# Kernel tuning notes

Measured on AMD Instinct MI355X. Metric: run time of the kernel, lower is better.

Reference implementation:

```python
import jax, jax.numpy as jnp
import numpy as np

N, E, G = 16384, 131072, 32
EPS = 1e-5


def seg_sum(x, ids, n):
    return jax.ops.segment_sum(x, ids, num_segments=n)


def seg_max(x, ids, n):
    return jax.ops.segment_max(x, ids, num_segments=n)


def gcn_conv(x, w, b, src, dst, n):
    # PyG GCNConv: add self loops, symmetric deg normalization
    loop = jnp.arange(n)
    s = jnp.concatenate([src, loop])
    d = jnp.concatenate([dst, loop])
    deg = seg_sum(jnp.ones_like(d, dtype=x.dtype), d, n)
    dis = jax.lax.rsqrt(deg)
    h = x @ w
    norm = (dis[s] * dis[d])[:, None]
    return seg_sum(h[s] * norm, d, n) + b


def sage_conv(x, wl, wr, b, src, dst, n):
    # mean aggregation of source features into target nodes
    cnt = seg_sum(jnp.ones_like(dst, dtype=x.dtype), dst, n)
    agg = seg_sum(x[src], dst, n) / jnp.maximum(cnt, 1.0)[:, None]
    return agg @ wl + x @ wr + b


def gat_conv(x, w, a_src, a_dst, b, src, dst, n, heads=4, ch=256):
    loop = jnp.arange(n)
    s = jnp.concatenate([src, loop])
    d = jnp.concatenate([dst, loop])
    h = (x @ w).reshape(n, heads, ch)            # [N,H,C]
    es = jnp.sum(h * a_src, axis=-1)             # [N,H]
    ed = jnp.sum(h * a_dst, axis=-1)             # [N,H]
    e = jax.nn.leaky_relu(es[s] + ed[d], 0.2)    # [E2,H]
    m = seg_max(e, d, n)
    ex = jnp.exp(e - m[d])
    z = seg_sum(ex, d, n)
    alpha = ex / z[d]                            # softmax over incoming edges
    out = seg_sum(h[s] * alpha[:, :, None], d, n)  # [N,H,C]
    return out.mean(axis=1) + b                  # concat=False -> head mean


def batchnorm(x, g, b):
    mu = x.mean(axis=0)
    var = x.var(axis=0)
    return (x - mu) * jax.lax.rsqrt(var + EPS) * g + b


def setup_inputs() -> dict:
    key = jax.random.key(0)
    ks = jax.random.split(key, 16)
    def w(k, shape, fan_in):
        return jax.random.normal(k, shape, jnp.float32) * (1.0 / np.sqrt(fan_in))
    return {
        "x": jax.random.uniform(ks[0], (N, 5), jnp.float32),
        "edge_index": jax.random.randint(ks[1], (2, E), 0, N),
        "batch": jnp.sort(jax.random.randint(ks[2], (N,), 0, G)),
        "gcn1_w": w(ks[3], (5, 64), 5), "gcn1_b": jnp.zeros((64,), jnp.float32),
        "sage_wl": w(ks[4], (64, 128), 64), "sage_wr": w(ks[5], (64, 128), 64),
        "sage_b": jnp.zeros((128,), jnp.float32),
        "gat_w": w(ks[6], (128, 1024), 128),
        "gat_asrc": w(ks[7], (4, 256), 256), "gat_adst": w(ks[8], (4, 256), 256),
        "gat_b": jnp.zeros((256,), jnp.float32),
        "gcn4_w": w(ks[9], (256, 512), 256), "gcn4_b": jnp.zeros((512,), jnp.float32),
        "bn1_g": jnp.ones((64,), jnp.float32), "bn1_b": jnp.zeros((64,), jnp.float32),
        "bn2_g": jnp.ones((128,), jnp.float32), "bn2_b": jnp.zeros((128,), jnp.float32),
        "bn3_g": jnp.ones((256,), jnp.float32), "bn3_b": jnp.zeros((256,), jnp.float32),
        "bn4_g": jnp.ones((512,), jnp.float32), "bn4_b": jnp.zeros((512,), jnp.float32),
        "fc_w": w(ks[10], (1024, 1024), 1024), "fc_b": jnp.zeros((1024,), jnp.float32),
    }


def reference(x, edge_index, batch, gcn1_w, gcn1_b, sage_wl, sage_wr, sage_b,
              gat_w, gat_asrc, gat_adst, gat_b, gcn4_w, gcn4_b,
              bn1_g, bn1_b, bn2_g, bn2_b, bn3_g, bn3_b, bn4_g, bn4_b,
              fc_w, fc_b):
    src, dst = edge_index[0], edge_index[1]
    n = x.shape[0]
    h = jax.nn.relu(batchnorm(gcn_conv(x, gcn1_w, gcn1_b, src, dst, n), bn1_g, bn1_b))
    h = jax.nn.relu(batchnorm(sage_conv(h, sage_wl, sage_wr, sage_b, src, dst, n), bn2_g, bn2_b))
    h = jax.nn.relu(batchnorm(gat_conv(h, gat_w, gat_asrc, gat_adst, gat_b, src, dst, n), bn3_g, bn3_b))
    h = jax.nn.relu(batchnorm(gcn_conv(h, gcn4_w, gcn4_b, src, dst, n), bn4_g, bn4_b))
    # global mean / max pooling over graphs in the batch
    cnt = seg_sum(jnp.ones((n,), h.dtype), batch, G)
    mean_p = seg_sum(h, batch, G) / jnp.maximum(cnt, 1.0)[:, None]
    max_p = seg_max(h, batch, G)
    max_p = jnp.where(cnt[:, None] > 0, max_p, 0.0)
    pooled = jnp.concatenate([mean_p, max_p], axis=1)  # [G,1024]
    return pooled @ fc_w + fc_b
```

## Files before the change

### kernel.cpp

```cpp
#include <hip/hip_runtime.h>

#define N_ 16384
#define E_ 131072
#define G_ 32
#define EPSF 1e-5f

typedef unsigned short bf16u;
typedef __attribute__((ext_vector_type(8))) short s8v;
typedef __attribute__((ext_vector_type(4))) float f4v;

__device__ __forceinline__ bf16u f2bf(float v) {
    union { float f; unsigned u; } x; x.f = v;
    unsigned r = x.u + 0x7FFF + ((x.u >> 16) & 1);
    return (bf16u)(r >> 16);
}
__device__ __forceinline__ float bf2f(bf16u u) {
    union { unsigned u; float f; } x; x.u = (unsigned)u << 16;
    return x.f;
}

static const size_t OFF_INDEG = 0;
static const size_t OFF_BNS   = 65536;
static const size_t OFF_BNQ   = 131072;
static const size_t OFF_POOL  = 196608;
static const size_t OFF_GB    = 327680;
static const size_t OFF_CNT   = 327816;
static const size_t OFF_MSET  = 327936;
static const size_t OFF_ROWS  = 327936;
static const size_t OFF_CURSOR= 393728;
static const size_t OFF_CSR   = 459264;
static const size_t OFF_DIS   = 983552;
static const size_t OFF_ES    = 1049088;
static const size_t OFF_ED    = 1311232;
static const size_t OFF_PART  = 1573376;
static const size_t OFF_BN1C  = 1578496;
static const size_t OFF_XA    = 1786624;
static const size_t OFF_AB    = 5980928;
static const size_t OFF_H2P   = 10175232;
static const size_t OFF_H2B   = 14369536;
static const size_t OFF_H3B   = 18563840;
static const size_t OFF_AGG   = 35328768;
static const size_t OFF_XA4B  = 52105984;
static const size_t OFF_WT1   = 68883200;
static const size_t OFF_WT2   = 69145344;
static const size_t OFF_WT3   = 69407488;
static const size_t OFF_H4B   = 69440256;
static const size_t OFF_VES   = 86479616;
static const size_t OFF_VED   = 86481664;

__global__ __launch_bounds__(1024) void k_scan(const int* __restrict__ indeg,
                                               int* __restrict__ rows,
                                               int* __restrict__ cursor,
                                               float* __restrict__ dis) {
    __shared__ int wtot[16];
    int t = threadIdx.x;
    int lane = t & 63, wave = t >> 6;
    int base = t * 16;
    int local[16];
    int s = 0;
#pragma unroll
    for (int i = 0; i < 16; ++i) {
        local[i] = indeg[base + i]; s += local[i];
        dis[base + i] = rsqrtf((float)local[i] + 1.0f);
    }
    int own = s;
#pragma unroll
    for (int off = 1; off < 64; off <<= 1) {
        int v = __shfl_up(s, off, 64);
        if (lane >= off) s += v;
    }
    if (lane == 63) wtot[wave] = s;
    __syncthreads();
    if (wave == 0) {
        int v = (lane < 16) ? wtot[lane] : 0;
#pragma unroll
        for (int off = 1; off < 16; off <<= 1) {
            int u = __shfl_up(v, off, 64);
            if (lane >= off) v += u;
        }
        if (lane < 16) wtot[lane] = v;
    }
    __syncthreads();
    int run = s - own + (wave > 0 ? wtot[wave - 1] : 0);
#pragma unroll
    for (int i = 0; i < 16; ++i) {
        rows[base + i] = run; cursor[base + i] = run; run += local[i];
    }
    if (t == 1023) rows[N_] = run;
}

__global__ void k_fill(const int* __restrict__ src, const int* __restrict__ dst,
                       int* __restrict__ cursor, int* __restrict__ csr) {
    int e = blockIdx.x * 256 + threadIdx.x;
    if (e < E_) {
        int p = atomicAdd(&cursor[dst[e]], 1);
        csr[p] = src[e];
    }
}

__global__ void k_wconv_all(const float* __restrict__ gat_w,
                            const float* __restrict__ gcn4_w,
                            const float* __restrict__ wl, const float* __restrict__ wr,
                            const int* __restrict__ batch,
                            const float* __restrict__ gat_as,
                            const float* __restrict__ gat_ad,
                            const int* __restrict__ dstE,
                            bf16u* __restrict__ wT1, bf16u* __restrict__ wT2,
                            bf16u* __restrict__ wT3, int* __restrict__ gb,
                            float* __restrict__ ves, float* __restrict__ ved,
                            int* __restrict__ indeg) {
    int idx = blockIdx.x * 256 + threadIdx.x;
    if (idx < 131072) {
        int k = idx >> 10, col = idx & 1023;
        int h = col >> 8, c = col & 255;
        wT1[(size_t)c * 512 + h * 128 + k] = f2bf(0.25f * gat_w[idx]);
    } else if (idx < 262144) {
        int j = idx - 131072;
        int k = j >> 9, m = j & 511;
        wT2[m * 256 + k] = f2bf(gcn4_w[j]);
    } else if (idx < 270336) {
        int j = idx - 262144;
        int k = j >> 7, m = j & 127;
        wT3[m * 128 + k] = f2bf(wl[j]);
    } else if (idx < 278528) {
        int j = idx - 270336;
        int k = j >> 7, m = j & 127;
        wT3[m * 128 + 64 + k] = f2bf(wr[j]);
    } else if (idx < 278592) {
        int g = idx - 278528;
        if (g > G_) return;
        if (g == G_) { gb[G_] = N_; return; }
        int lo = 0, hi = N_;
        while (lo < hi) { int mid = (lo + hi) >> 1; if (batch[mid] < g) lo = mid + 1; else hi = mid; }
        gb[g] = lo;
    } else if (idx < 279104) {
        int j = idx - 278592;
        int h = j >> 7, k = j & 127;
        float s = 0.f;
        for (int c = 0; c < 256; ++c)
            s += gat_w[(size_t)k * 1024 + h*256 + c] * gat_as[h*256 + c];
        ves[j] = s;
    } else if (idx < 279616) {
        int j = idx - 279104;
        int h = j >> 7, k = j & 127;
        float s = 0.f;
        for (int c = 0; c < 256; ++c)
            s += gat_w[(size_t)k * 1024 + h*256 + c] * gat_ad[h*256 + c];
        ved[j] = s;
    } else if (idx < 410688) {
        int e = idx - 279616;
        atomicAdd(&indeg[dstE[e]], 1);
    }
}

__global__ __launch_bounds__(256) void k_gcn1x(const float* __restrict__ x,
                                               const float* __restrict__ dis,
                                               const int* __restrict__ rows,
                                               const int* __restrict__ csr,
                                               float* __restrict__ xa) {
    int wave = threadIdx.x >> 6, lane = threadIdx.x & 63;
    int i = blockIdx.x * 4 + wave;
    float a0=0,a1=0,a2=0,a3=0,a4=0;
    int e0 = rows[i], e1 = rows[i+1];
    for (int e = e0 + lane; e < e1; e += 64) {
        int s = csr[e];
        float wt = dis[s];
        a0 += x[s*5+0]*wt; a1 += x[s*5+1]*wt; a2 += x[s*5+2]*wt;
        a3 += x[s*5+3]*wt; a4 += x[s*5+4]*wt;
    }
#pragma unroll
    for (int off = 32; off > 0; off >>= 1) {
        a0 += __shfl_xor(a0, off, 64); a1 += __shfl_xor(a1, off, 64);
        a2 += __shfl_xor(a2, off, 64); a3 += __shfl_xor(a3, off, 64);
        a4 += __shfl_xor(a4, off, 64);
    }
    float di = dis[i];
    float v0 = di*(a0 + di*x[i*5+0]);
    float v1 = di*(a1 + di*x[i*5+1]);
    float v2 = di*(a2 + di*x[i*5+2]);
    float v3 = di*(a3 + di*x[i*5+3]);
    float v4 = di*(a4 + di*x[i*5+4]);
    if (lane < 5) {
        float v = lane == 0 ? v0 : lane == 1 ? v1 : lane == 2 ? v2 : lane == 3 ? v3 : v4;
        xa[(size_t)i*8 + lane] = v;
    }
}

__global__ __launch_bounds__(256) void k_xstats(const float* __restrict__ xa,
                                                float* __restrict__ partial,
                                                int* __restrict__ cnt,
                                                const float* __restrict__ w,
                                                const float* __restrict__ b,
                                                const float* __restrict__ bng,
                                                const float* __restrict__ bnb,
                                                float* __restrict__ sc,
                                                float* __restrict__ sh) {
    __shared__ float wsum[80];
    __shared__ int lastFlag;
    int t = threadIdx.x;
    int tid = blockIdx.x * 256 + t;
    float v0 = xa[(size_t)tid*8+0], v1 = xa[(size_t)tid*8+1], v2 = xa[(size_t)tid*8+2];
    float v3 = xa[(size_t)tid*8+3], v4 = xa[(size_t)tid*8+4];
    float m[20];
    m[0]=v0; m[1]=v1; m[2]=v2; m[3]=v3; m[4]=v4;
    m[5]=v0*v0;  m[6]=v0*v1;  m[7]=v0*v2;  m[8]=v0*v3;  m[9]=v0*v4;
    m[10]=v1*v1; m[11]=v1*v2; m[12]=v1*v3; m[13]=v1*v4;
    m[14]=v2*v2; m[15]=v2*v3; m[16]=v2*v4;
    m[17]=v3*v3; m[18]=v3*v4;
    m[19]=v4*v4;
#pragma unroll
    for (int off = 32; off > 0; off >>= 1)
#pragma unroll
        for (int j = 0; j < 20; ++j) m[j] += __shfl_xor(m[j], off, 64);
    int wave = t >> 6, lane = t & 63;
    if (lane == 0)
#pragma unroll
        for (int j = 0; j < 20; ++j) wsum[wave*20 + j] = m[j];
    __syncthreads();
    if (t < 20) {
        partial[blockIdx.x * 20 + t] = wsum[t] + wsum[20+t] + wsum[40+t] + wsum[60+t];
        __threadfence();
    }
    __syncthreads();
    if (t == 0) lastFlag = (atomicAdd(cnt, 1) == 63);
    __syncthreads();
    if (!lastFlag || t >= 64) return;
    int l = t;
    const float invN = 1.0f / (float)N_;
    float mm[20];
#pragma unroll
    for (int j = 0; j < 20; ++j) {
        float v = partial[l*20 + j];
#pragma unroll
        for (int off = 32; off > 0; off >>= 1) v += __shfl_xor(v, off, 64);
        mm[j] = v * invN;
    }
    int c = l;
    float wc0 = w[c], wc1 = w[64+c], wc2 = w[128+c], wc3 = w[192+c], wc4 = w[256+c];
    float mu = b[c] + mm[0]*wc0 + mm[1]*wc1 + mm[2]*wc2 + mm[3]*wc3 + mm[4]*wc4;
    float var = 0.f;
    var += (mm[5]  - mm[0]*mm[0]) * wc0*wc0;
    var += (mm[6]  - mm[0]*mm[1]) * wc0*wc1 * 2.f;
    var += (mm[7]  - mm[0]*mm[2]) * wc0*wc2 * 2.f;
    var += (mm[8]  - mm[0]*mm[3]) * wc0*wc3 * 2.f;
    var += (mm[9]  - mm[0]*mm[4]) * wc0*wc4 * 2.f;
    var += (mm[10] - mm[1]*mm[1]) * wc1*wc1;
    var += (mm[11] - mm[1]*mm[2]) * wc1*wc2 * 2.f;
    var += (mm[12] - mm[1]*mm[3]) * wc1*wc3 * 2.f;
    var += (mm[13] - mm[1]*mm[4]) * wc1*wc4 * 2.f;
    var += (mm[14] - mm[2]*mm[2]) * wc2*wc2;
    var += (mm[15] - mm[2]*mm[3]) * wc2*wc3 * 2.f;
    var += (mm[16] - mm[2]*mm[4]) * wc2*wc4 * 2.f;
    var += (mm[17] - mm[3]*mm[3]) * wc3*wc3;
    var += (mm[18] - mm[3]*mm[4]) * wc3*wc4 * 2.f;
    var += (mm[19] - mm[4]*mm[4]) * wc4*wc4;
    float scale = rsqrtf(var + EPSF) * bng[c];
    sc[c] = scale;
    sh[c] = fmaf(b[c], scale, bnb[c] - mu * scale);
}

__global__ __launch_bounds__(256) void k_sage_l1(const float* __restrict__ xa,
                                                 const float* __restrict__ sc,
                                                 const float* __restrict__ sh,
                                                 const float* __restrict__ w,
                                                 const int* __restrict__ rows,
                                                 const int* __restrict__ csr,
                                                 bf16u* __restrict__ ab) {
    int wave = threadIdx.x >> 6, lane = threadIdx.x & 63;
    int i = blockIdx.x * 4 + wave;
    int c = lane;
    float wc0 = w[c], wc1 = w[64+c], wc2 = w[128+c], wc3 = w[192+c], wc4 = w[256+c];
    float scale = sc[c], base = sh[c];
    {
        float4 p = *(const float4*)&xa[(size_t)i*8];
        float p4 = xa[(size_t)i*8 + 4];
        float t = p.x*wc0 + p.y*wc1 + p.z*wc2 + p.w*wc3 + p4*wc4;
        float v = fmaf(t, scale, base); v = v > 0.f ? v : 0.f;
        ab[(size_t)i*128 + 64 + c] = f2bf(v);
    }
    int e0 = rows[i], e1 = rows[i+1];
    float s = 0.f;
    int e = e0;
    for (; e + 3 < e1; e += 4) {
        int s0 = csr[e], s1 = csr[e+1], s2 = csr[e+2], s3 = csr[e+3];
        float4 q0 = *(const float4*)&xa[(size_t)s0*8]; float r0 = xa[(size_t)s0*8+4];
        float4 q1 = *(const float4*)&xa[(size_t)s1*8]; float r1 = xa[(size_t)s1*8+4];
        float4 q2 = *(const float4*)&xa[(size_t)s2*8]; float r2 = xa[(size_t)s2*8+4];
        float4 q3 = *(const float4*)&xa[(size_t)s3*8]; float r3 = xa[(size_t)s3*8+4];
        float t0 = q0.x*wc0 + q0.y*wc1 + q0.z*wc2 + q0.w*wc3 + r0*wc4;
        float t1 = q1.x*wc0 + q1.y*wc1 + q1.z*wc2 + q1.w*wc3 + r1*wc4;
        float t2 = q2.x*wc0 + q2.y*wc1 + q2.z*wc2 + q2.w*wc3 + r2*wc4;
        float t3 = q3.x*wc0 + q3.y*wc1 + q3.z*wc2 + q3.w*wc3 + r3*wc4;
        float v;
        v = fmaf(t0, scale, base); s += v > 0.f ? v : 0.f;
        v = fmaf(t1, scale, base); s += v > 0.f ? v : 0.f;
        v = fmaf(t2, scale, base); s += v > 0.f ? v : 0.f;
        v = fmaf(t3, scale, base); s += v > 0.f ? v : 0.f;
    }
    for (; e < e1; ++e) {
        int sI = csr[e];
        float4 q = *(const float4*)&xa[(size_t)sI*8]; float r = xa[(size_t)sI*8+4];
        float t = q.x*wc0 + q.y*wc1 + q.z*wc2 + q.w*wc3 + r*wc4;
        float v = fmaf(t, scale, base); s += v > 0.f ? v : 0.f;
    }
    ab[(size_t)i*128 + c] = f2bf(s / fmaxf((float)(e1 - e0), 1.0f));
}

__global__ __launch_bounds__(256) void k_gemm_mfma(const bf16u* __restrict__ A,
                                                   const bf16u* __restrict__ BT,
                                                   const float* __restrict__ bias,
                                                   bf16u* __restrict__ C,
                                                   float* __restrict__ sum,
                                                   float* __restrict__ sumsq,
                                                   int K, int M) {
    __shared__ bf16u As[128][40];
    __shared__ bf16u Bs[128][40];
    int tid = threadIdx.x;
    int wave = tid >> 6, lane = tid & 63;
    int wr = (wave >> 1) * 64, wc = (wave & 1) * 64;
    int row0 = blockIdx.y * 128, col0 = blockIdx.x * 128;
    f4v acc[4][4];
#pragma unroll
    for (int i = 0; i < 4; ++i)
#pragma unroll
        for (int j = 0; j < 4; ++j) acc[i][j] = (f4v)0.0f;

    int sr = tid >> 1;
    int sh = (tid & 1) * 16;
    int lr = lane & 15, lq = lane >> 4;

    for (int k0 = 0; k0 < K; k0 += 32) {
        const bf16u* ap = A + (size_t)(row0 + sr) * K + k0 + sh;
        *(uint4*)&As[sr][sh]     = *(const uint4*)ap;
        *(uint4*)&As[sr][sh + 8] = *(const uint4*)(ap + 8);
        const bf16u* bp = BT + (size_t)(col0 + sr) * K + k0 + sh;
        *(uint4*)&Bs[sr][sh]     = *(const uint4*)bp;
        *(uint4*)&Bs[sr][sh + 8] = *(const uint4*)(bp + 8);
        __syncthreads();
        s8v af[4], bfr[4];
#pragma unroll
        for (int i = 0; i < 4; ++i)
            af[i] = *(const s8v*)&As[wr + i*16 + lr][lq*8];
#pragma unroll
        for (int j = 0; j < 4; ++j)
            bfr[j] = *(const s8v*)&Bs[wc + j*16 + lr][lq*8];
#pragma unroll
        for (int i = 0; i < 4; ++i)
#pragma unroll
            for (int j = 0; j < 4; ++j)
                acc[i][j] = __builtin_amdgcn_mfma_f32_16x16x32_bf16(af[i], bfr[j], acc[i][j], 0, 0, 0);
        __syncthreads();
    }

    int slot = (blockIdx.y & 7) << 9;
#pragma unroll
    for (int j = 0; j < 4; ++j) {
        int col = col0 + wc + j*16 + lr;
        float bv = bias ? bias[col] : 0.f;
        float s = 0.f, q = 0.f;
#pragma unroll
        for (int i = 0; i < 4; ++i) {
#pragma unroll
            for (int r = 0; r < 4; ++r) {
                float v = acc[i][j][r] + bv;
                int row = row0 + wr + i*16 + lq*4 + r;
                C[(size_t)row * M + col] = f2bf(v);
                s += v; q += v*v;
            }
        }
        if (sum) {
            s += __shfl_xor(s, 16, 64); q += __shfl_xor(q, 16, 64);
            s += __shfl_xor(s, 32, 64); q += __shfl_xor(q, 32, 64);
            if (lq == 0) { atomicAdd(&sum[slot + col], s); atomicAdd(&sumsq[slot + col], q); }
        }
    }
}

__global__ __launch_bounds__(256) void k_bn_apply2b_attn(
        const bf16u* __restrict__ hp, const float* __restrict__ sum,
        const float* __restrict__ sumsq, const float* __restrict__ g,
        const float* __restrict__ b, const float* __restrict__ ves,
        const float* __restrict__ ved, bf16u* __restrict__ hb,
        float* __restrict__ es, float* __restrict__ ed) {
    int wave = threadIdx.x >> 6, lane = threadIdx.x & 63;
    int i = blockIdx.x * 4 + wave;
    int c = lane * 2;
    const float invN = 1.0f / (float)N_;
    float sx=0.f, sy=0.f, qx=0.f, qy=0.f;
#pragma unroll
    for (int s8 = 0; s8 < 8; ++s8) {
        float2 a = *(const float2*)&sum[s8*512 + c];
        float2 d = *(const float2*)&sumsq[s8*512 + c];
        sx += a.x; sy += a.y; qx += d.x; qy += d.y;
    }
    float2 gg = *(const float2*)&g[c];
    float2 bb = *(const float2*)&b[c];
    float mu0 = sx*invN, mu1 = sy*invN;
    float sc0 = rsqrtf(qx*invN - mu0*mu0 + EPSF)*gg.x, sh0 = bb.x - mu0*sc0;
    float sc1 = rsqrtf(qy*invN - mu1*mu1 + EPSF)*gg.y, sh1 = bb.y - mu1*sc1;
    unsigned pv = *(const unsigned*)&hp[(size_t)i*128 + c];
    float v0 = bf2f((bf16u)(pv & 0xFFFF));
    float v1 = bf2f((bf16u)(pv >> 16));
    v0 = fmaf(v0, sc0, sh0); v0 = v0 > 0.f ? v0 : 0.f;
    v1 = fmaf(v1, sc1, sh1); v1 = v1 > 0.f ? v1 : 0.f;
    unsigned ow = (unsigned)f2bf(v0) | ((unsigned)f2bf(v1) << 16);
    *(unsigned*)&hb[(size_t)i*128 + c] = ow;
    float vs[4], vd[4];
#pragma unroll
    for (int h = 0; h < 4; ++h) {
        float2 a = *(const float2*)&ves[h*128 + c];
        float2 d = *(const float2*)&ved[h*128 + c];
        vs[h] = v0*a.x + v1*a.y;
        vd[h] = v0*d.x + v1*d.y;
    }
#pragma unroll
    for (int off = 32; off > 0; off >>= 1) {
#pragma unroll
        for (int h = 0; h < 4; ++h) {
            vs[h] += __shfl_xor(vs[h], off, 64);
            vd[h] += __shfl_xor(vd[h], off, 64);
        }
    }
    if (lane == 0) {
        *(float4*)&es[i*4] = make_float4(vs[0], vs[1], vs[2], vs[3]);
        *(float4*)&ed[i*4] = make_float4(vd[0], vd[1], vd[2], vd[3]);
    }
}

__global__ __launch_bounds__(256) void k_gat_agg2(const bf16u* __restrict__ h2b,
                                                  const float* __restrict__ es,
                                                  const float* __restrict__ ed,
                                                  const int* __restrict__ rows,
                                                  const int* __restrict__ csr,
                                                  bf16u* __restrict__ agg) {
    int wave = threadIdx.x >> 6, lane = threadIdx.x & 63;
    int i = blockIdx.x * 4 + wave;
    int c = lane * 2;
    float4 edv = *(const float4*)&ed[i*4];
    float4 sv  = *(const float4*)&es[i*4];
    int e0 = rows[i], e1 = rows[i+1];
    float e, m0, m1, m2, m3;
    e = sv.x + edv.x; m0 = e >= 0.f ? e : 0.2f*e;
    e = sv.y + edv.y; m1 = e >= 0.f ? e : 0.2f*e;
    e = sv.z + edv.z; m2 = e >= 0.f ? e : 0.2f*e;
    e = sv.w + edv.w; m3 = e >= 0.f ? e : 0.2f*e;
    float z0, z1, z2, z3;
    float a00, a01, a10, a11, a20, a21, a30, a31;
    {
        z0 = 1.f; z1 = 1.f; z2 = 1.f; z3 = 1.f;
        unsigned pv = *(const unsigned*)&h2b[(size_t)i*128 + c];
        float v0 = bf2f((bf16u)(pv & 0xFFFF)), v1 = bf2f((bf16u)(pv >> 16));
        a00 = v0; a01 = v1; a10 = v0; a11 = v1;
        a20 = v0; a21 = v1; a30 = v0; a31 = v1;
    }
#define GEXP(Q, EDC, M) __expf(fminf(((Q) + (EDC) >= 0.f ? (Q) + (EDC) : 0.2f*((Q) + (EDC))) - (M), 80.f))
    int ee = e0;
    for (; ee + 3 < e1; ee += 4) {
        int s0 = csr[ee], s1 = csr[ee+1], s2i = csr[ee+2], s3i = csr[ee+3];
        float4 q0 = *(const float4*)&es[s0*4];
        float4 q1 = *(const float4*)&es[s1*4];
        float4 q2 = *(const float4*)&es[s2i*4];
        float4 q3 = *(const float4*)&es[s3i*4];
        unsigned p0 = *(const unsigned*)&h2b[(size_t)s0*128 + c];
        unsigned p1 = *(const unsigned*)&h2b[(size_t)s1*128 + c];
        unsigned p2 = *(const unsigned*)&h2b[(size_t)s2i*128 + c];
        unsigned p3 = *(const unsigned*)&h2b[(size_t)s3i*128 + c];
        float v0, v1, ex;
        v0 = bf2f((bf16u)(p0 & 0xFFFF)); v1 = bf2f((bf16u)(p0 >> 16));
        ex = GEXP(q0.x, edv.x, m0); z0 += ex; a00 = fmaf(ex, v0, a00); a01 = fmaf(ex, v1, a01);
        ex = GEXP(q0.y, edv.y, m1); z1 += ex; a10 = fmaf(ex, v0, a10); a11 = fmaf(ex, v1, a11);
        ex = GEXP(q0.z, edv.z, m2); z2 += ex; a20 = fmaf(ex, v0, a20); a21 = fmaf(ex, v1, a21);
        ex = GEXP(q0.w, edv.w, m3); z3 += ex; a30 = fmaf(ex, v0, a30); a31 = fmaf(ex, v1, a31);
        v0 = bf2f((bf16u)(p1 & 0xFFFF)); v1 = bf2f((bf16u)(p1 >> 16));
        ex = GEXP(q1.x, edv.x, m0); z0 += ex; a00 = fmaf(ex, v0, a00); a01 = fmaf(ex, v1, a01);
        ex = GEXP(q1.y, edv.y, m1); z1 += ex; a10 = fmaf(ex, v0, a10); a11 = fmaf(ex, v1, a11);
        ex = GEXP(q1.z, edv.z, m2); z2 += ex; a20 = fmaf(ex, v0, a20); a21 = fmaf(ex, v1, a21);
        ex = GEXP(q1.w, edv.w, m3); z3 += ex; a30 = fmaf(ex, v0, a30); a31 = fmaf(ex, v1, a31);
        v0 = bf2f((bf16u)(p2 & 0xFFFF)); v1 = bf2f((bf16u)(p2 >> 16));
        ex = GEXP(q2.x, edv.x, m0); z0 += ex; a00 = fmaf(ex, v0, a00); a01 = fmaf(ex, v1, a01);
        ex = GEXP(q2.y, edv.y, m1); z1 += ex; a10 = fmaf(ex, v0, a10); a11 = fmaf(ex, v1, a11);
        ex = GEXP(q2.z, edv.z, m2); z2 += ex; a20 = fmaf(ex, v0, a20); a21 = fmaf(ex, v1, a21);
        ex = GEXP(q2.w, edv.w, m3); z3 += ex; a30 = fmaf(ex, v0, a30); a31 = fmaf(ex, v1, a31);
        v0 = bf2f((bf16u)(p3 & 0xFFFF)); v1 = bf2f((bf16u)(p3 >> 16));
        ex = GEXP(q3.x, edv.x, m0); z0 += ex; a00 = fmaf(ex, v0, a00); a01 = fmaf(ex, v1, a01);
        ex = GEXP(q3.y, edv.y, m1); z1 += ex; a10 = fmaf(ex, v0, a10); a11 = fmaf(ex, v1, a11);
        ex = GEXP(q3.z, edv.z, m2); z2 += ex; a20 = fmaf(ex, v0, a20); a21 = fmaf(ex, v1, a21);
        ex = GEXP(q3.w, edv.w, m3); z3 += ex; a30 = fmaf(ex, v0, a30); a31 = fmaf(ex, v1, a31);
    }
    for (; ee < e1; ++ee) {
        int s = csr[ee];
        float4 s2 = *(const float4*)&es[s*4];
        unsigned pv = *(const unsigned*)&h2b[(size_t)s*128 + c];
        float v0 = bf2f((bf16u)(pv & 0xFFFF)), v1 = bf2f((bf16u)(pv >> 16));
        float ex;
        ex = GEXP(s2.x, edv.x, m0); z0 += ex; a00 = fmaf(ex, v0, a00); a01 = fmaf(ex, v1, a01);
        ex = GEXP(s2.y, edv.y, m1); z1 += ex; a10 = fmaf(ex, v0, a10); a11 = fmaf(ex, v1, a11);
        ex = GEXP(s2.z, edv.z, m2); z2 += ex; a20 = fmaf(ex, v0, a20); a21 = fmaf(ex, v1, a21);
        ex = GEXP(s2.w, edv.w, m3); z3 += ex; a30 = fmaf(ex, v0, a30); a31 = fmaf(ex, v1, a31);
    }
#undef GEXP
    size_t base = (size_t)i * 512 + c;
    float r; unsigned ow;
    r = 1.f/z0; ow = (unsigned)f2bf(a00*r) | ((unsigned)f2bf(a01*r) << 16);
    *(unsigned*)&agg[base]       = ow;
    r = 1.f/z1; ow = (unsigned)f2bf(a10*r) | ((unsigned)f2bf(a11*r) << 16);
    *(unsigned*)&agg[base + 128] = ow;
    r = 1.f/z2; ow = (unsigned)f2bf(a20*r) | ((unsigned)f2bf(a21*r) << 16);
    *(unsigned*)&agg[base + 256] = ow;
    r = 1.f/z3; ow = (unsigned)f2bf(a30*r) | ((unsigned)f2bf(a31*r) << 16);
    *(unsigned*)&agg[base + 384] = ow;
}

__global__ __launch_bounds__(256) void k_gcn4_agg(const bf16u* __restrict__ h3b,
                                                  const float* __restrict__ dis,
                                                  const int* __restrict__ rows,
                                                  const int* __restrict__ csr,
                                                  const float* __restrict__ sum,
                                                  const float* __restrict__ sumsq,
                                                  const float* __restrict__ g,
                                                  const float* __restrict__ b,
                                                  bf16u* __restrict__ xab) {
    int wave = threadIdx.x >> 6, q = threadIdx.x & 63;
    int i = blockIdx.x * 4 + wave;
    int c = q * 4;
    const float invN = 1.0f / (float)N_;
    float4 sm = make_float4(0.f,0.f,0.f,0.f), sq = make_float4(0.f,0.f,0.f,0.f);
#pragma unroll
    for (int s8 = 0; s8 < 8; ++s8) {
        float4 a = *(const float4*)&sum[s8*512 + c];
        float4 d = *(const float4*)&sumsq[s8*512 + c];
        sm.x += a.x; sm.y += a.y; sm.z += a.z; sm.w += a.w;
        sq.x += d.x; sq.y += d.y; sq.z += d.z; sq.w += d.w;
    }
    float4 gg = *(const float4*)&g[c];
    float4 bb = *(const float4*)&b[c];
    float mu, sc0, sc1, sc2, sc3, sh0, sh1, sh2, sh3;
    mu = sm.x*invN; sc0 = rsqrtf(sq.x*invN - mu*mu + EPSF)*gg.x; sh0 = bb.x - mu*sc0;
    mu = sm.y*invN; sc1 = rsqrtf(sq.y*invN - mu*mu + EPSF)*gg.y; sh1 = bb.y - mu*sc1;
    mu = sm.z*invN; sc2 = rsqrtf(sq.z*invN - mu*mu + EPSF)*gg.z; sh2 = bb.z - mu*sc2;
    mu = sm.w*invN; sc3 = rsqrtf(sq.w*invN - mu*mu + EPSF)*gg.w; sh3 = bb.w - mu*sc3;
    float di = dis[i];
    float a0, a1, a2, a3;
    {
        ushort4 u = *(const ushort4*)(h3b + (size_t)i*256 + c);
        float v, dd = di * di;
        v = fmaf(bf2f(u.x), sc0, sh0); v = v > 0.f ? v : 0.f; a0 = v * dd;
        v = fmaf(bf2f(u.y), sc1, sh1); v = v > 0.f ? v : 0.f; a1 = v * dd;
        v = fmaf(bf2f(u.z), sc2, sh2); v = v > 0.f ? v : 0.f; a2 = v * dd;
        v = fmaf(bf2f(u.w), sc3, sh3); v = v > 0.f ? v : 0.f; a3 = v * dd;
    }
    int e0 = rows[i], e1 = rows[i+1];
    int e = e0;
    for (; e + 3 < e1; e += 4) {
        int s0 = csr[e], s1 = csr[e+1], s2i = csr[e+2], s3i = csr[e+3];
        float w0 = dis[s0] * di, w1 = dis[s1] * di, w2 = dis[s2i] * di, w3 = dis[s3i] * di;
        ushort4 u0 = *(const ushort4*)(h3b + (size_t)s0*256 + c);
        ushort4 u1 = *(const ushort4*)(h3b + (size_t)s1*256 + c);
        ushort4 u2 = *(const ushort4*)(h3b + (size_t)s2i*256 + c);
        ushort4 u3 = *(const ushort4*)(h3b + (size_t)s3i*256 + c);
        float v;
        v = fmaf(bf2f(u0.x), sc0, sh0); v = v > 0.f ? v : 0.f; a0 += v * w0;
        v = fmaf(bf2f(u0.y), sc1, sh1); v = v > 0.f ? v : 0.f; a1 += v * w0;
        v = fmaf(bf2f(u0.z), sc2, sh2); v = v > 0.f ? v : 0.f; a2 += v * w0;
        v = fmaf(bf2f(u0.w), sc3, sh3); v = v > 0.f ? v : 0.f; a3 += v * w0;
        v = fmaf(bf2f(u1.x), sc0, sh0); v = v > 0.f ? v : 0.f; a0 += v * w1;
        v = fmaf(bf2f(u1.y), sc1, sh1); v = v > 0.f ? v : 0.f; a1 += v * w1;
        v = fmaf(bf2f(u1.z), sc2, sh2); v = v > 0.f ? v : 0.f; a2 += v * w1;
        v = fmaf(bf2f(u1.w), sc3, sh3); v = v > 0.f ? v : 0.f; a3 += v * w1;
        v = fmaf(bf2f(u2.x), sc0, sh0); v = v > 0.f ? v : 0.f; a0 += v * w2;
        v = fmaf(bf2f(u2.y), sc1, sh1); v = v > 0.f ? v : 0.f; a1 += v * w2;
        v = fmaf(bf2f(u2.z), sc2, sh2); v = v > 0.f ? v : 0.f; a2 += v * w2;
        v = fmaf(bf2f(u2.w), sc3, sh3); v = v > 0.f ? v : 0.f; a3 += v * w2;
        v = fmaf(bf2f(u3.x), sc0, sh0); v = v > 0.f ? v : 0.f; a0 += v * w3;
        v = fmaf(bf2f(u3.y), sc1, sh1); v = v > 0.f ? v : 0.f; a1 += v * w3;
        v = fmaf(bf2f(u3.z), sc2, sh2); v = v > 0.f ? v : 0.f; a2 += v * w3;
        v = fmaf(bf2f(u3.w), sc3, sh3); v = v > 0.f ? v : 0.f; a3 += v * w3;
    }
    for (; e < e1; ++e) {
        int s = csr[e];
        float w = dis[s] * di;
        ushort4 u = *(const ushort4*)(h3b + (size_t)s*256 + c);
        float v;
        v = fmaf(bf2f(u.x), sc0, sh0); v = v > 0.f ? v : 0.f; a0 += v * w;
        v = fmaf(bf2f(u.y), sc1, sh1); v = v > 0.f ? v : 0.f; a1 += v * w;
        v = fmaf(bf2f(u.z), sc2, sh2); v = v > 0.f ? v : 0.f; a2 += v * w;
        v = fmaf(bf2f(u.w), sc3, sh3); v = v > 0.f ? v : 0.f; a3 += v * w;
    }
    ushort4 o;
    o.x = f2bf(a0); o.y = f2bf(a1); o.z = f2bf(a2); o.w = f2bf(a3);
    *(ushort4*)(xab + (size_t)i*256 + c) = o;
}

__global__ void k_pool(const bf16u* __restrict__ h4b, const int* __restrict__ gb,
                       const float* __restrict__ sum, const float* __restrict__ sumsq,
                       const float* __restrict__ g, const float* __restrict__ b,
                       const float* __restrict__ fcb,
                       float* __restrict__ pooled, float* __restrict__ out) {
    int bidx = blockIdx.x;
    int t = threadIdx.x;
    if (bidx >= 512) {
        int i = (bidx - 512) * 256 + t;
        out[i] = fcb[i & 1023];
        return;
    }
    int gi = bidx >> 4;
    int chunk = bidx & 15;
    const float invN = 1.0f / (float)N_;
    float su0=0.f, qq0=0.f, su1=0.f, qq1=0.f;
#pragma unroll
    for (int s8 = 0; s8 < 8; ++s8) {
        su0 += sum[s8*512 + t];       qq0 += sumsq[s8*512 + t];
        su1 += sum[s8*512 + 256 + t]; qq1 += sumsq[s8*512 + 256 + t];
    }
    float mu0 = su0 * invN;
    float sc0 = rsqrtf(qq0 * invN - mu0*mu0 + EPSF) * g[t];
    float sh0 = b[t] - mu0 * sc0;
    float mu1 = su1 * invN;
    float sc1 = rsqrtf(qq1 * invN - mu1*mu1 + EPSF) * g[t+256];
    float sh1 = b[t+256] - mu1 * sc1;
    int r0g = gb[gi], r1g = gb[gi+1];
    int n = r1g - r0g;
    if (n <= 0) return;
    int per = (n + 15) >> 4;
    int r0 = r0g + chunk * per;
    int r1 = min(r0 + per, r1g);
    if (r0 >= r1) return;
    float s0=0.f, s1=0.f, m0=0.f, m1=0.f;
    for (int r = r0; r < r1; ++r) {
        float v = fmaf(bf2f(h4b[(size_t)r*512 + t]), sc0, sh0);
        v = v > 0.f ? v : 0.f;
        s0 += v; m0 = fmaxf(m0, v);
        float w = fmaf(bf2f(h4b[(size_t)r*512 + 256 + t]), sc1, sh1);
        w = w > 0.f ? w : 0.f;
        s1 += w; m1 = fmaxf(m1, w);
    }
    atomicAdd(&pooled[gi*1024 + t], s0);
    atomicAdd(&pooled[gi*1024 + 256 + t], s1);
    atomicMax((int*)&pooled[gi*1024 + 512 + t],  __float_as_int(m0));
    atomicMax((int*)&pooled[gi*1024 + 768 + t],  __float_as_int(m1));
}

#define FCKZ 16
#define FCKC (1024 / FCKZ)

__global__ __launch_bounds__(256) void k_fc2(const float* __restrict__ pooled,
                                             const float* __restrict__ w,
                                             const int* __restrict__ gb,
                                             float* __restrict__ out) {
    __shared__ float pr[FCKC];
    int g = blockIdx.x;
    int z = blockIdx.y;
    int t = threadIdx.x;
    int k0 = z * FCKC;
    if (t < FCKC) {
        float scale = (z < 8) ? 1.0f / fmaxf((float)(gb[g+1] - gb[g]), 1.0f) : 1.0f;
        pr[t] = pooled[g * 1024 + k0 + t] * scale;
    }
    __syncthreads();
    int m0 = t * 4;
    float ax = 0.f, ay = 0.f, az = 0.f, aw = 0.f;
#pragma unroll 8
    for (int k = 0; k < FCKC; ++k) {
        const float4 wv = *(const float4*)&w[(size_t)(k0 + k) * 1024 + m0];
        float p = pr[k];
        ax += p * wv.x; ay += p * wv.y; az += p * wv.z; aw += p * wv.w;
    }
    atomicAdd(&out[g * 1024 + m0 + 0], ax);
    atomicAdd(&out[g * 1024 + m0 + 1], ay);
    atomicAdd(&out[g * 1024 + m0 + 2], az);
    atomicAdd(&out[g * 1024 + m0 + 3], aw);
}

extern "C" void kernel_launch(void* const* d_in, const int* in_sizes, int n_in,
                              void* d_out, int out_size, void* d_ws, size_t ws_size,
                              hipStream_t stream) {
    (void)in_sizes; (void)n_in; (void)out_size; (void)ws_size;
    const float* x       = (const float*)d_in[0];
    const int*   ei      = (const int*)d_in[1];
    const int*   batch   = (const int*)d_in[2];
    const float* gcn1_w  = (const float*)d_in[3];
    const float* gcn1_b  = (const float*)d_in[4];
    const float* sage_wl = (const float*)d_in[5];
    const float* sage_wr = (const float*)d_in[6];
    const float* sage_b  = (const float*)d_in[7];
    const float* gat_w   = (const float*)d_in[8];
    const float* gat_as  = (const float*)d_in[9];
    const float* gat_ad  = (const float*)d_in[10];
    const float* gat_b   = (const float*)d_in[11];
    const float* gcn4_w  = (const float*)d_in[12];
    const float* gcn4_b  = (const float*)d_in[13];
    const float* bn1_g   = (const float*)d_in[14];
    const float* bn1_b   = (const float*)d_in[15];
    const float* bn2_g   = (const float*)d_in[16];
    const float* bn2_b   = (const float*)d_in[17];
    const float* bn3_g   = (const float*)d_in[18];
    const float* bn3_b   = (const float*)d_in[19];
    const float* bn4_g   = (const float*)d_in[20];
    const float* bn4_b   = (const float*)d_in[21];
    const float* fc_w    = (const float*)d_in[22];
    const float* fc_b    = (const float*)d_in[23];
    float* out = (float*)d_out;

    char* w8 = (char*)d_ws;
    int*   indeg  = (int*)(w8 + OFF_INDEG);
    float* bns    = (float*)(w8 + OFF_BNS);
    float* bnq    = (float*)(w8 + OFF_BNQ);
    float* pooled = (float*)(w8 + OFF_POOL);
    int*   gb     = (int*)(w8 + OFF_GB);
    int*   cnt    = (int*)(w8 + OFF_CNT);
    int*   rows   = (int*)(w8 + OFF_ROWS);
    int*   cursor = (int*)(w8 + OFF_CURSOR);
    int*   csr    = (int*)(w8 + OFF_CSR);
    float* dis    = (float*)(w8 + OFF_DIS);
    float* es     = (float*)(w8 + OFF_ES);
    float* ed     = (float*)(w8 + OFF_ED);
    float* part   = (float*)(w8 + OFF_PART);
    float* bn1sc  = (float*)(w8 + OFF_BN1C);
    float* bn1sh  = (float*)(w8 + OFF_BN1C + 256);
    float* xa     = (float*)(w8 + OFF_XA);
    bf16u* ab     = (bf16u*)(w8 + OFF_AB);
    bf16u* h2p    = (bf16u*)(w8 + OFF_H2P);
    bf16u* h2b    = (bf16u*)(w8 + OFF_H2B);
    bf16u* h3b    = (bf16u*)(w8 + OFF_H3B);
    bf16u* agg    = (bf16u*)(w8 + OFF_AGG);
    bf16u* xa4b   = (bf16u*)(w8 + OFF_XA4B);
    bf16u* wT1    = (bf16u*)(w8 + OFF_WT1);
    bf16u* wT2    = (bf16u*)(w8 + OFF_WT2);
    bf16u* wT3    = (bf16u*)(w8 + OFF_WT3);
    bf16u* h4b    = (bf16u*)(w8 + OFF_H4B);
    float* ves    = (float*)(w8 + OFF_VES);
    float* ved    = (float*)(w8 + OFF_VED);

    const int* srcE = ei;
    const int* dstE = ei + E_;

    hipMemsetAsync(w8, 0, OFF_MSET, stream);
    k_wconv_all<<<1605, 256, 0, stream>>>(gat_w, gcn4_w, sage_wl, sage_wr, batch,
                                          gat_as, gat_ad, dstE,
                                          wT1, wT2, wT3, gb, ves, ved, indeg);
    k_scan<<<1, 1024, 0, stream>>>(indeg, rows, cursor, dis);
    k_fill<<<E_/256, 256, 0, stream>>>(srcE, dstE, cursor, csr);

    k_gcn1x<<<N_/4, 256, 0, stream>>>(x, dis, rows, csr, xa);
    k_xstats<<<64, 256, 0, stream>>>(xa, part, cnt, gcn1_w, gcn1_b, bn1_g, bn1_b,
                                     bn1sc, bn1sh);
    k_sage_l1<<<N_/4, 256, 0, stream>>>(xa, bn1sc, bn1sh, gcn1_w, rows, csr, ab);

    {
        dim3 grid(1, N_/128);
        k_gemm_mfma<<<grid, 256, 0, stream>>>(ab, wT3, sage_b, h2p,
                                              bns + 4096, bnq + 4096, 128, 128);
    }
    k_bn_apply2b_attn<<<N_/4, 256, 0, stream>>>(h2p, bns + 4096, bnq + 4096, bn2_g, bn2_b,
                                                ves, ved, h2b, es, ed);

    k_gat_agg2<<<N_/4, 256, 0, stream>>>(h2b, es, ed, rows, csr, agg);
    {
        dim3 grid(256/128, N_/128);
        k_gemm_mfma<<<grid, 256, 0, stream>>>(agg, wT1, gat_b, h3b,
                                              bns + 8192, bnq + 8192, 512, 256);
    }

    k_gcn4_agg<<<N_/4, 256, 0, stream>>>(h3b, dis, rows, csr, bns + 8192, bnq + 8192,
                                         bn3_g, bn3_b, xa4b);
    {
        dim3 grid(512/128, N_/128);
        k_gemm_mfma<<<grid, 256, 0, stream>>>(xa4b, wT2, gcn4_b, h4b,
                                              bns + 12288, bnq + 12288, 256, 512);
    }

    k_pool<<<640, 256, 0, stream>>>(h4b, gb, bns + 12288, bnq + 12288, bn4_g, bn4_b,
                                    fc_b, pooled, out);

    {
        dim3 grid(G_, FCKZ);
        k_fc2<<<grid, 256, 0, stream>>>(pooled, fc_w, gb, out);
    }
}
```

Baseline: 285.5 us.

## Fuse indegree count with scan, CSR fill with weight prep, stats into gcn1

Merges five front-end kernels into three. The indegree atomic count now carries the prefix scan in its last block, selected by an atomic counter. The CSR fill shares a launch with the weight conversion. The BN1 statistics reduction moves into the gcn1 aggregation kernel using a last-block pattern. The intent is to remove launch and inter-kernel gaps. In exchange the scan runs in a single 256-thread block doing serial 64-element loops, and the stats finalisation reads 4096 partials in one block.

New measurement: 394.0 us. 1.38x slower.

```diff
diff --git a/kernel.cpp b/kernel.cpp
--- a/kernel.cpp
+++ b/kernel.cpp
@@ -25,6 +25,7 @@
 static const size_t OFF_POOL  = 196608;
 static const size_t OFF_GB    = 327680;
 static const size_t OFF_CNT   = 327816;
+static const size_t OFF_CNT2  = 327820;
 static const size_t OFF_MSET  = 327936;
 static const size_t OFF_ROWS  = 327936;
 static const size_t OFF_CURSOR= 393728;
@@ -33,83 +34,84 @@
 static const size_t OFF_ES    = 1049088;
 static const size_t OFF_ED    = 1311232;
 static const size_t OFF_PART  = 1573376;
-static const size_t OFF_BN1C  = 1578496;
-static const size_t OFF_XA    = 1786624;
-static const size_t OFF_AB    = 5980928;
-static const size_t OFF_H2P   = 10175232;
-static const size_t OFF_H2B   = 14369536;
-static const size_t OFF_H3B   = 18563840;
-static const size_t OFF_AGG   = 35328768;
-static const size_t OFF_XA4B  = 52105984;
-static const size_t OFF_WT1   = 68883200;
-static const size_t OFF_WT2   = 69145344;
-static const size_t OFF_WT3   = 69407488;
-static const size_t OFF_H4B   = 69440256;
-static const size_t OFF_VES   = 86479616;
-static const size_t OFF_VED   = 86481664;
-
-__global__ __launch_bounds__(1024) void k_scan(const int* __restrict__ indeg,
+static const size_t OFF_BN1C  = 1901056;
+static const size_t OFF_XA    = 1901568;
+static const size_t OFF_AB    = 2425856;
+static const size_t OFF_H2P   = 6620160;
+static const size_t OFF_H2B   = 10814464;
+static const size_t OFF_H3B   = 15008768;
+static const size_t OFF_AGG   = 23397376;
+static const size_t OFF_XA4B  = 40174592;
+static const size_t OFF_WT1   = 48563200;
+static const size_t OFF_WT2   = 48825344;
+static const size_t OFF_WT3   = 49087488;
+static const size_t OFF_H4B   = 49120256;
+static const size_t OFF_VES   = 65897472;
+static const size_t OFF_VED   = 65899520;
+
+__global__ __launch_bounds__(256) void k_indeg(const int* __restrict__ dstE,
+                                               int* __restrict__ indeg,
+                                               int* __restrict__ cnt,
                                                int* __restrict__ rows,
                                                int* __restrict__ cursor,
                                                float* __restrict__ dis) {
-    __shared__ int wtot[16];
+    __shared__ int lpart[256];
+    __shared__ int lastFlag;
     int t = threadIdx.x;
-    int lane = t & 63, wave = t >> 6;
-    int base = t * 16;
-    int local[16];
+    int e = blockIdx.x * 256 + t;
+    atomicAdd(&indeg[dstE[e]], 1);
+    __threadfence();
+    __syncthreads();
+    if (t == 0) lastFlag = (atomicAdd(cnt, 1) == 511);
+    __syncthreads();
+    if (!lastFlag) return;
+    __threadfence();
+    int base = t * 64;
     int s = 0;
-#pragma unroll
-    for (int i = 0; i < 16; ++i) {
-        local[i] = indeg[base + i]; s += local[i];
-        dis[base + i] = rsqrtf((float)local[i] + 1.0f);
-    }
-    int own = s;
-#pragma unroll
-    for (int off = 1; off < 64; off <<= 1) {
-        int v = __shfl_up(s, off, 64);
-        if (lane >= off) s += v;
-    }
-    if (lane == 63) wtot[wave] = s;
-    __syncthreads();
-    if (wave == 0) {
-        int v = (lane < 16) ? wtot[lane] : 0;
-#pragma unroll
-        for (int off = 1; off < 16; off <<= 1) {
-            int u = __shfl_up(v, off, 64);
-            if (lane >= off) v += u;
-        }
-        if (lane < 16) wtot[lane] = v;
-    }
-    __syncthreads();
-    int run = s - own + (wave > 0 ? wtot[wave - 1] : 0);
-#pragma unroll
-    for (int i = 0; i < 16; ++i) {
-        rows[base + i] = run; cursor[base + i] = run; run += local[i];
-    }
-    if (t == 1023) rows[N_] = run;
-}
-
-__global__ void k_fill(const int* __restrict__ src, const int* __restrict__ dst,
-                       int* __restrict__ cursor, int* __restrict__ csr) {
-    int e = blockIdx.x * 256 + threadIdx.x;
-    if (e < E_) {
-        int p = atomicAdd(&cursor[dst[e]], 1);
-        csr[p] = src[e];
-    }
-}
-
-__global__ void k_wconv_all(const float* __restrict__ gat_w,
-                            const float* __restrict__ gcn4_w,
-                            const float* __restrict__ wl, const float* __restrict__ wr,
-                            const int* __restrict__ batch,
-                            const float* __restrict__ gat_as,
-                            const float* __restrict__ gat_ad,
-                            const int* __restrict__ dstE,
-                            bf16u* __restrict__ wT1, bf16u* __restrict__ wT2,
-                            bf16u* __restrict__ wT3, int* __restrict__ gb,
-                            float* __restrict__ ves, float* __restrict__ ved,
-                            int* __restrict__ indeg) {
-    int idx = blockIdx.x * 256 + threadIdx.x;
+    for (int i = 0; i < 64; ++i) s += indeg[base + i];
+    lpart[t] = s;
+    __syncthreads();
+    for (int off = 1; off < 256; off <<= 1) {
+        int v = (t >= off) ? lpart[t - off] : 0;
+        __syncthreads();
+        lpart[t] += v;
+        __syncthreads();
+    }
+    int run = (t == 0) ? 0 : lpart[t - 1];
+    for (int i = 0; i < 64; ++i) {
+        int d = indeg[base + i];
+        rows[base + i] = run; cursor[base + i] = run;
+        dis[base + i] = rsqrtf((float)d + 1.0f);
+        run += d;
+    }
+    if (t == 255) rows[N_] = run;
+}
+
+__global__ __launch_bounds__(256) void k_fillw(const int* __restrict__ srcE,
+                                               const int* __restrict__ dstE,
+                                               int* __restrict__ cursor,
+                                               int* __restrict__ csr,
+                                               const float* __restrict__ gat_w,
+                                               const float* __restrict__ gcn4_w,
+                                               const float* __restrict__ wl,
+                                               const float* __restrict__ wr,
+                                               const int* __restrict__ batch,
+                                               const float* __restrict__ gat_as,
+                                               const float* __restrict__ gat_ad,
+                                               bf16u* __restrict__ wT1,
+                                               bf16u* __restrict__ wT2,
+                                               bf16u* __restrict__ wT3,
+                                               int* __restrict__ gb,
+                                               float* __restrict__ ves,
+                                               float* __restrict__ ved) {
+    int bid = blockIdx.x, t = threadIdx.x;
+    if (bid < 512) {
+        int e = bid * 256 + t;
+        int p = atomicAdd(&cursor[dstE[e]], 1);
+        csr[p] = srcE[e];
+        return;
+    }
+    int idx = (bid - 512) * 256 + t;
     if (idx < 131072) {
         int k = idx >> 10, col = idx & 1023;
         int h = col >> 8, c = col & 255;
@@ -147,9 +149,6 @@
         for (int c = 0; c < 256; ++c)
             s += gat_w[(size_t)k * 1024 + h*256 + c] * gat_ad[h*256 + c];
         ved[j] = s;
-    } else if (idx < 410688) {
-        int e = idx - 279616;
-        atomicAdd(&indeg[dstE[e]], 1);
     }
 }
 
@@ -157,8 +156,19 @@
                                                const float* __restrict__ dis,
                                                const int* __restrict__ rows,
                                                const int* __restrict__ csr,
-                                               float* __restrict__ xa) {
-    int wave = threadIdx.x >> 6, lane = threadIdx.x & 63;
+                                               float* __restrict__ xa,
+                                               float* __restrict__ partial,
+                                               int* __restrict__ cnt2,
+                                               const float* __restrict__ w,
+                                               const float* __restrict__ b,
+                                               const float* __restrict__ bng,
+                                               const float* __restrict__ bnb,
+                                               float* __restrict__ sc,
+                                               float* __restrict__ sh) {
+    __shared__ float wm[80];
+    __shared__ int lastFlag;
+    int t = threadIdx.x;
+    int wave = t >> 6, lane = t & 63;
     int i = blockIdx.x * 4 + wave;
     float a0=0,a1=0,a2=0,a3=0,a4=0;
     int e0 = rows[i], e1 = rows[i+1];
@@ -184,79 +194,70 @@
         float v = lane == 0 ? v0 : lane == 1 ? v1 : lane == 2 ? v2 : lane == 3 ? v3 : v4;
         xa[(size_t)i*8 + lane] = v;
     }
-}
-
-__global__ __launch_bounds__(256) void k_xstats(const float* __restrict__ xa,
-                                                float* __restrict__ partial,
-                                                int* __restrict__ cnt,
-                                                const float* __restrict__ w,
-                                                const float* __restrict__ b,
-                                                const float* __restrict__ bng,
-                                                const float* __restrict__ bnb,
-                                                float* __restrict__ sc,
-                                                float* __restrict__ sh) {
-    __shared__ float wsum[80];
-    __shared__ int lastFlag;
-    int t = threadIdx.x;
-    int tid = blockIdx.x * 256 + t;
-    float v0 = xa[(size_t)tid*8+0], v1 = xa[(size_t)tid*8+1], v2 = xa[(size_t)tid*8+2];
-    float v3 = xa[(size_t)tid*8+3], v4 = xa[(size_t)tid*8+4];
-    float m[20];
-    m[0]=v0; m[1]=v1; m[2]=v2; m[3]=v3; m[4]=v4;
-    m[5]=v0*v0;  m[6]=v0*v1;  m[7]=v0*v2;  m[8]=v0*v3;  m[9]=v0*v4;
-    m[10]=v1*v1; m[11]=v1*v2; m[12]=v1*v3; m[13]=v1*v4;
-    m[14]=v2*v2; m[15]=v2*v3; m[16]=v2*v4;
-    m[17]=v3*v3; m[18]=v3*v4;
-    m[19]=v4*v4;
+    if (lane == 0) {
+        wm[wave*20 + 0] = v0;  wm[wave*20 + 1] = v1;  wm[wave*20 + 2] = v2;
+        wm[wave*20 + 3] = v3;  wm[wave*20 + 4] = v4;
+        wm[wave*20 + 5] = v0*v0;  wm[wave*20 + 6] = v0*v1;  wm[wave*20 + 7] = v0*v2;
+        wm[wave*20 + 8] = v0*v3;  wm[wave*20 + 9] = v0*v4;
+        wm[wave*20 +10] = v1*v1;  wm[wave*20 +11] = v1*v2;  wm[wave*20 +12] = v1*v3;
+        wm[wave*20 +13] = v1*v4;
+        wm[wave*20 +14] = v2*v2;  wm[wave*20 +15] = v2*v3;  wm[wave*20 +16] = v2*v4;
+        wm[wave*20 +17] = v3*v3;  wm[wave*20 +18] = v3*v4;
+        wm[wave*20 +19] = v4*v4;
+    }
+    __syncthreads();
+    if (t < 20) {
+        partial[blockIdx.x * 20 + t] = wm[t] + wm[20+t] + wm[40+t] + wm[60+t];
+        __threadfence();
+    }
+    __syncthreads();
+    if (t == 0) lastFlag = (atomicAdd(cnt2, 1) == 4095);
+    __syncthreads();
+    if (!lastFlag) return;
+    __threadfence();
+    float mm[20];
+#pragma unroll
+    for (int j = 0; j < 20; ++j) mm[j] = 0.f;
+    for (int r = t; r < 4096; r += 256) {
+#pragma unroll
+        for (int j = 0; j < 20; ++j) mm[j] += partial[r*20 + j];
+    }
 #pragma unroll
     for (int off = 32; off > 0; off >>= 1)
 #pragma unroll
-        for (int j = 0; j < 20; ++j) m[j] += __shfl_xor(m[j], off, 64);
-    int wave = t >> 6, lane = t & 63;
+        for (int j = 0; j < 20; ++j) mm[j] += __shfl_xor(mm[j], off, 64);
+    __syncthreads();
     if (lane == 0)
 #pragma unroll
-        for (int j = 0; j < 20; ++j) wsum[wave*20 + j] = m[j];
-    __syncthreads();
-    if (t < 20) {
-        partial[blockIdx.x * 20 + t] = wsum[t] + wsum[20+t] + wsum[40+t] + wsum[60+t];
-        __threadfence();
-    }
-    __syncthreads();
-    if (t == 0) lastFlag = (atomicAdd(cnt, 1) == 63);
-    __syncthreads();
-    if (!lastFlag || t >= 64) return;
-    int l = t;
-    const float invN = 1.0f / (float)N_;
-    float mm[20];
-#pragma unroll
-    for (int j = 0; j < 20; ++j) {
-        float v = partial[l*20 + j];
-#pragma unroll
-        for (int off = 32; off > 0; off >>= 1) v += __shfl_xor(v, off, 64);
-        mm[j] = v * invN;
-    }
-    int c = l;
-    float wc0 = w[c], wc1 = w[64+c], wc2 = w[128+c], wc3 = w[192+c], wc4 = w[256+c];
-    float mu = b[c] + mm[0]*wc0 + mm[1]*wc1 + mm[2]*wc2 + mm[3]*wc3 + mm[4]*wc4;
-    float var = 0.f;
-    var += (mm[5]  - mm[0]*mm[0]) * wc0*wc0;
-    var += (mm[6]  - mm[0]*mm[1]) * wc0*wc1 * 2.f;
-    var += (mm[7]  - mm[0]*mm[2]) * wc0*wc2 * 2.f;
-    var += (mm[8]  - mm[0]*mm[3]) * wc0*wc3 * 2.f;
-    var += (mm[9]  - mm[0]*mm[4]) * wc0*wc4 * 2.f;
-    var += (mm[10] - mm[1]*mm[1]) * wc1*wc1;
-    var += (mm[11] - mm[1]*mm[2]) * wc1*wc2 * 2.f;
-    var += (mm[12] - mm[1]*mm[3]) * wc1*wc3 * 2.f;
-    var += (mm[13] - mm[1]*mm[4]) * wc1*wc4 * 2.f;
-    var += (mm[14] - mm[2]*mm[2]) * wc2*wc2;
-    var += (mm[15] - mm[2]*mm[3]) * wc2*wc3 * 2.f;
-    var += (mm[16] - mm[2]*mm[4]) * wc2*wc4 * 2.f;
-    var += (mm[17] - mm[3]*mm[3]) * wc3*wc3;
-    var += (mm[18] - mm[3]*mm[4]) * wc3*wc4 * 2.f;
-    var += (mm[19] - mm[4]*mm[4]) * wc4*wc4;
-    float scale = rsqrtf(var + EPSF) * bng[c];
-    sc[c] = scale;
-    sh[c] = fmaf(b[c], scale, bnb[c] - mu * scale);
+        for (int j = 0; j < 20; ++j) wm[wave*20 + j] = mm[j];
+    __syncthreads();
+    if (t < 20) wm[t] = (wm[t] + wm[20+t] + wm[40+t] + wm[60+t]) * (1.0f/(float)N_);
+    __syncthreads();
+    if (t < 64) {
+        int c = t;
+        float M0=wm[0], M1=wm[1], M2=wm[2], M3=wm[3], M4=wm[4];
+        float wc0 = w[c], wc1 = w[64+c], wc2 = w[128+c], wc3 = w[192+c], wc4 = w[256+c];
+        float mu = b[c] + M0*wc0 + M1*wc1 + M2*wc2 + M3*wc3 + M4*wc4;
+        float var = 0.f;
+        var += (wm[5]  - M0*M0) * wc0*wc0;
+        var += (wm[6]  - M0*M1) * wc0*wc1 * 2.f;
+        var += (wm[7]  - M0*M2) * wc0*wc2 * 2.f;
+        var += (wm[8]  - M0*M3) * wc0*wc3 * 2.f;
+        var += (wm[9]  - M0*M4) * wc0*wc4 * 2.f;
+        var += (wm[10] - M1*M1) * wc1*wc1;
+        var += (wm[11] - M1*M2) * wc1*wc2 * 2.f;
+        var += (wm[12] - M1*M3) * wc1*wc3 * 2.f;
+        var += (wm[13] - M1*M4) * wc1*wc4 * 2.f;
+        var += (wm[14] - M2*M2) * wc2*wc2;
+        var += (wm[15] - M2*M3) * wc2*wc3 * 2.f;
+        var += (wm[16] - M2*M4) * wc2*wc4 * 2.f;
+        var += (wm[17] - M3*M3) * wc3*wc3;
+        var += (wm[18] - M3*M4) * wc3*wc4 * 2.f;
+        var += (wm[19] - M4*M4) * wc4*wc4;
+        float scale = rsqrtf(var + EPSF) * bng[c];
+        sc[c] = scale;
+        sh[c] = fmaf(b[c], scale, bnb[c] - mu * scale);
+    }
 }
 
 __global__ __launch_bounds__(256) void k_sage_l1(const float* __restrict__ xa,
@@ -708,6 +709,7 @@
     float* pooled = (float*)(w8 + OFF_POOL);
     int*   gb     = (int*)(w8 + OFF_GB);
     int*   cnt    = (int*)(w8 + OFF_CNT);
+    int*   cnt2   = (int*)(w8 + OFF_CNT2);
     int*   rows   = (int*)(w8 + OFF_ROWS);
     int*   cursor = (int*)(w8 + OFF_CURSOR);
     int*   csr    = (int*)(w8 + OFF_CSR);
@@ -735,15 +737,13 @@
     const int* dstE = ei + E_;
 
     hipMemsetAsync(w8, 0, OFF_MSET, stream);
-    k_wconv_all<<<1605, 256, 0, stream>>>(gat_w, gcn4_w, sage_wl, sage_wr, batch,
-                                          gat_as, gat_ad, dstE,
-                                          wT1, wT2, wT3, gb, ves, ved, indeg);
-    k_scan<<<1, 1024, 0, stream>>>(indeg, rows, cursor, dis);
-    k_fill<<<E_/256, 256, 0, stream>>>(srcE, dstE, cursor, csr);
-
-    k_gcn1x<<<N_/4, 256, 0, stream>>>(x, dis, rows, csr, xa);
-    k_xstats<<<64, 256, 0, stream>>>(xa, part, cnt, gcn1_w, gcn1_b, bn1_g, bn1_b,
-                                     bn1sc, bn1sh);
+    k_indeg<<<512, 256, 0, stream>>>(dstE, indeg, cnt, rows, cursor, dis);
+    k_fillw<<<1605, 256, 0, stream>>>(srcE, dstE, cursor, csr, gat_w, gcn4_w,
+                                      sage_wl, sage_wr, batch, gat_as, gat_ad,
+                                      wT1, wT2, wT3, gb, ves, ved);
+
+    k_gcn1x<<<N_/4, 256, 0, stream>>>(x, dis, rows, csr, xa, part, cnt2,
+                                      gcn1_w, gcn1_b, bn1_g, bn1_b, bn1sc, bn1sh);
     k_sage_l1<<<N_/4, 256, 0, stream>>>(xa, bn1sc, bn1sh, gcn1_w, rows, csr, ab);
 
     {
```
